# Kernel tuning notes

Hardware: AMD Instinct MI355X
Metric: run time of the kernel (lower is better)

Reference implementation:

```python
import jax, jax.numpy as jnp
import numpy as np

NPOINT, RADIUS, NSAMPLE = 1024, 0.2, 32
BN_EPS = 1e-5


def fps(xyz_bn3, npoint):
    # xyz_bn3: (B, N, 3) -> (B, npoint) int32 indices; starts from point 0 like the CUDA ext.
    def one(x):
        N = x.shape[0]
        def step(carry, _):
            dist, last = carry
            d = jnp.sum((x - x[last]) ** 2, axis=-1)
            dist = jnp.minimum(dist, d)
            nxt = jnp.argmax(dist).astype(jnp.int32)
            return (dist, nxt), nxt
        init = (jnp.full((N,), 1e10, dtype=x.dtype), jnp.int32(0))
        _, rest = jax.lax.scan(step, init, None, length=npoint - 1)
        return jnp.concatenate([jnp.zeros((1,), jnp.int32), rest])
    return jax.vmap(one)(xyz_bn3)


def ball_query(radius, nsample, xyz, new_xyz):
    # xyz: (B, N, 3), new_xyz: (B, S, 3) -> (B, S, nsample) int32
    # First nsample points within radius; pad slots with the first found index.
    N = xyz.shape[1]
    d2 = jnp.sum((new_xyz[:, :, None, :] - xyz[:, None, :, :]) ** 2, axis=-1)  # (B,S,N)
    ar = jnp.arange(N, dtype=jnp.int32)
    cand = jnp.where(d2 <= radius * radius, ar, N)
    idx = jnp.sort(cand, axis=-1)[..., :nsample]
    first = idx[..., :1]
    return jnp.where(idx == N, first, idx)


def group(features, idx):
    # features: (B, C, N), idx: (B, S, K) -> (B, C, S, K)
    return jax.vmap(lambda f, i: f[:, i])(features, idx)


def conv_bn_relu(x, w, b, g, bt, rm, rv):
    # x: (B, Cin, S, K); 1x1 conv + eval-mode BatchNorm + ReLU
    y = jnp.einsum('oc,bcsk->bosk', w, x) + b[:, None, None]
    y = g[:, None, None] * (y - rm[:, None, None]) * jax.lax.rsqrt(rv[:, None, None] + BN_EPS) + bt[:, None, None]
    return jax.nn.relu(y)


def setup_inputs() -> dict:
    key = jax.random.key(0)
    ks = jax.random.split(key, 16)
    B, N, D = 8, 4096, 64
    mlp = [64, 64, 128]
    cin = 3 + D
    inp = {
        'xyz': jax.random.uniform(ks[0], (B, 3, N), dtype=jnp.float32),
        'points': jax.random.normal(ks[1], (B, D, N), dtype=jnp.float32),
    }
    last = cin
    kidx = 2
    for i, co in enumerate(mlp):
        inp[f'w{i}'] = jax.random.normal(ks[kidx], (co, last), dtype=jnp.float32) * (1.0 / np.sqrt(last)); kidx += 1
        inp[f'b{i}'] = jax.random.normal(ks[kidx], (co,), dtype=jnp.float32) * 0.01; kidx += 1
        inp[f'g{i}'] = jax.random.uniform(ks[kidx], (co,), dtype=jnp.float32) + 0.5; kidx += 1
        inp[f'bt{i}'] = jax.random.normal(ks[kidx], (co,), dtype=jnp.float32) * 0.01; kidx += 1
        inp[f'rm{i}'] = jnp.zeros((co,), dtype=jnp.float32)
        inp[f'rv{i}'] = jnp.ones((co,), dtype=jnp.float32)
        last = co
    return inp


def reference(xyz, points, w0, b0, g0, bt0, rm0, rv0, w1, b1, g1, bt1, rm1, rv1, w2, b2, g2, bt2, rm2, rv2):
    xyz_t = jnp.transpose(xyz, (0, 2, 1))  # (B, N, 3)
    fps_idx = fps(xyz_t, NPOINT)  # (B, S)
    new_xyz = jax.vmap(lambda f, i: f[:, i])(xyz, fps_idx)  # (B, 3, S)
    idx = ball_query(RADIUS, NSAMPLE, xyz_t, jnp.transpose(new_xyz, (0, 2, 1)))  # (B, S, K)
    grouped_xyz = group(xyz, idx) - new_xyz[..., None]  # (B, 3, S, K)
    grouped_pts = group(points, idx)  # (B, D, S, K)
    feat = jnp.concatenate([grouped_xyz, grouped_pts], axis=1)  # (B, 3+D, S, K)
    feat = conv_bn_relu(feat, w0, b0, g0, bt0, rm0, rv0)
    feat = conv_bn_relu(feat, w1, b1, g1, bt1, rm1, rv1)
    feat = conv_bn_relu(feat, w2, b2, g2, bt2, rm2, rv2)
    new_features = jnp.max(feat, axis=-1)  # (B, 128, S)
    return new_xyz, new_features
```

## Files before the change

kernel.cpp:

```cpp
#include <hip/hip_runtime.h>
#include <cstdint>
#include <cstddef>

#define NPOINT 1024
#define NSAMPLE 32
#define BATCH 8
#define NPTS 4096
#define DFEAT 64
#define CIN 67
#define C1 64
#define C2 64
#define C3 128
#define BN_EPS 1e-5f

__device__ __forceinline__ float wave64_max_bcast(float v) {
    int x;
    x = __builtin_amdgcn_update_dpp(0, __float_as_int(v), 0x111, 0xf, 0xf, true);
    v = fmaxf(v, __int_as_float(x));
    x = __builtin_amdgcn_update_dpp(0, __float_as_int(v), 0x112, 0xf, 0xf, true);
    v = fmaxf(v, __int_as_float(x));
    x = __builtin_amdgcn_update_dpp(0, __float_as_int(v), 0x114, 0xf, 0xf, true);
    v = fmaxf(v, __int_as_float(x));
    x = __builtin_amdgcn_update_dpp(0, __float_as_int(v), 0x118, 0xf, 0xf, true);
    v = fmaxf(v, __int_as_float(x));
    x = __builtin_amdgcn_update_dpp(0, __float_as_int(v), 0x142, 0xf, 0xf, true);
    v = fmaxf(v, __int_as_float(x));
    x = __builtin_amdgcn_update_dpp(0, __float_as_int(v), 0x143, 0xf, 0xf, true);
    v = fmaxf(v, __int_as_float(x));
    return __int_as_float(__builtin_amdgcn_readlane(__float_as_int(v), 63));
}

__global__ __launch_bounds__(512) void fps_kernel(const float* __restrict__ xyz,
                                                  float* __restrict__ dout) {
    const int b = blockIdx.x;
    const float* xb = xyz + (size_t)b * 3 * NPTS;
    float* ox = dout + (size_t)b * 3 * NPOINT;

    __shared__ float sx[NPTS], sy[NPTS], sz[NPTS];
    __shared__ unsigned long long redk[2][8];

    const int t = threadIdx.x;
    const int wv = t >> 6, lane = t & 63;
    for (int j = t; j < NPTS; j += 512) {
        sx[j] = xb[j];
        sy[j] = xb[NPTS + j];
        sz[j] = xb[2 * NPTS + j];
    }
    __syncthreads();

    constexpr int PT = NPTS / 512;
    float px[PT], py[PT], pz[PT], dist[PT];
    const int base = t * PT;
#pragma unroll
    for (int u = 0; u < PT; ++u) {
        px[u] = sx[base + u];
        py[u] = sy[base + u];
        pz[u] = sz[base + u];
        dist[u] = 1e10f;
    }

    int last = 0;
    float o0x = 0.f, o0y = 0.f, o0z = 0.f;
    float o1x = 0.f, o1y = 0.f, o1z = 0.f;

    for (int s = 1; s < NPOINT; ++s) {
        const float cx = sx[last], cy = sy[last], cz = sz[last];
        if (s - 1 == t)       { o0x = cx; o0y = cy; o0z = cz; }
        if (s - 1 == t + 512) { o1x = cx; o1y = cy; o1z = cz; }

        float bv = 0.0f;
#pragma unroll
        for (int u = 0; u < PT; ++u) {
            float dx = __fsub_rn(px[u], cx);
            float dy = __fsub_rn(py[u], cy);
            float dz = __fsub_rn(pz[u], cz);
            float d = __fadd_rn(__fadd_rn(__fmul_rn(dx, dx), __fmul_rn(dy, dy)),
                                __fmul_rn(dz, dz));
            float nd = fminf(dist[u], d);
            dist[u] = nd;
            bv = fmaxf(bv, nd);
        }
        const float wmax = wave64_max_bcast(bv);
        int li = 0;
        if (bv == wmax) {
#pragma unroll
            for (int u = PT - 1; u >= 0; --u)
                if (dist[u] == wmax) li = base + u;
        }
        const unsigned long long m = __ballot(bv == wmax);
        const int fl = __builtin_ctzll(m);
        const int wbi = __builtin_amdgcn_readlane(li, fl);

        if ((t & 63) == 0) {
            redk[s & 1][wv] =
                ((unsigned long long)__float_as_uint(wmax) << 32) |
                (unsigned)(0xFFFFFFFFu - (unsigned)wbi);
        }
        __syncthreads();
        unsigned long long gk = redk[s & 1][0];
#pragma unroll
        for (int w = 1; w < 8; ++w) {
            unsigned long long k2 = redk[s & 1][w];
            if (k2 > gk) gk = k2;
        }
        last = (int)(0xFFFFFFFFu - (unsigned)(gk & 0xFFFFFFFFull));
    }

    {
        const float cx = sx[last], cy = sy[last], cz = sz[last];
        if (t == 511) { o1x = cx; o1y = cy; o1z = cz; }
    }

    ox[t] = o0x;
    ox[NPOINT + t] = o0y;
    ox[2 * NPOINT + t] = o0z;
    ox[512 + t] = o1x;
    ox[NPOINT + 512 + t] = o1y;
    ox[2 * NPOINT + 512 + t] = o1z;
}

__global__ __launch_bounds__(256) void transpose_pts(const float* __restrict__ pts,
                                                     float* __restrict__ ptsT) {
    __shared__ float tile[64][65];
    const int b = blockIdx.x / (NPTS / 64);
    const int n0 = (blockIdx.x % (NPTS / 64)) * 64;
    const int t = threadIdx.x;
    const int nl = t & 63, cq = t >> 6;
    const float* pb = pts + (size_t)b * DFEAT * NPTS;
#pragma unroll
    for (int i = 0; i < 16; ++i) {
        int c = i * 4 + cq;
        tile[c][nl] = pb[(size_t)c * NPTS + n0 + nl];
    }
    __syncthreads();
    float* ob = ptsT + (size_t)b * NPTS * DFEAT;
    const int cl = t & 63, nq = t >> 6;
#pragma unroll
    for (int i = 0; i < 16; ++i) {
        int n = i * 4 + nq;
        ob[(size_t)(n0 + n) * DFEAT + cl] = tile[cl][n];
    }
}

__global__ __launch_bounds__(256) void ballquery_kernel(const float* __restrict__ xyz,
                                                        const float* __restrict__ dout,
                                                        int* __restrict__ idx) {
    const int wv = threadIdx.x >> 6, lane = threadIdx.x & 63;
    const int sg = blockIdx.x * 4 + wv;
    const int b = sg / NPOINT, s = sg % NPOINT;
    const float* xb = xyz + (size_t)b * 3 * NPTS;
    const float* nx = dout + (size_t)b * 3 * NPOINT;
    const float cx = nx[s], cy = nx[NPOINT + s], cz = nx[2 * NPOINT + s];
    int* ob = idx + (size_t)sg * NSAMPLE;
    const float r2 = 0.04f;

    int cnt = 0;
    int first = -1;
    for (int tch = 0; tch < NPTS / 64 && cnt < NSAMPLE; ++tch) {
        const int j = tch * 64 + lane;
        float dx = __fsub_rn(cx, xb[j]);
        float dy = __fsub_rn(cy, xb[NPTS + j]);
        float dz = __fsub_rn(cz, xb[2 * NPTS + j]);
        float d2 = __fadd_rn(__fadd_rn(__fmul_rn(dx, dx), __fmul_rn(dy, dy)),
                             __fmul_rn(dz, dz));
        unsigned long long mask = __ballot(d2 <= r2);
        while (mask && cnt < NSAMPLE) {
            int bit = __builtin_ctzll(mask);
            int pj = tch * 64 + bit;
            if (cnt == 0) first = pj;
            if (lane == 0) ob[cnt] = pj;
            cnt++;
            mask &= mask - 1;
        }
    }
    if (lane == 0) {
        for (int r = cnt; r < NSAMPLE; ++r) ob[r] = first;
    }
}

template <int TRANSPOSED>
__global__ __launch_bounds__(256) void mlp_kernel(
    const float* __restrict__ xyz, const float* __restrict__ pts,
    const int* __restrict__ idx, const float* __restrict__ dnew,
    const float* __restrict__ w0, const float* __restrict__ b0,
    const float* __restrict__ g0, const float* __restrict__ bt0,
    const float* __restrict__ rm0, const float* __restrict__ rv0,
    const float* __restrict__ w1, const float* __restrict__ b1,
    const float* __restrict__ g1, const float* __restrict__ bt1,
    const float* __restrict__ rm1, const float* __restrict__ rv1,
    const float* __restrict__ w2, const float* __restrict__ b2,
    const float* __restrict__ g2, const float* __restrict__ bt2,
    const float* __restrict__ rm2, const float* __restrict__ rv2,
    float* __restrict__ outf) {
    __shared__ float ylds[64][256];
    const int t = threadIdx.x;
    const int k = t & 31, sl = t >> 5;
    const int b = blockIdx.x >> 7;
    const int s = (blockIdx.x & 127) * 8 + sl;
    const int p = idx[((size_t)(b * NPOINT + s)) * NSAMPLE + k];

    const float* xb = xyz + (size_t)b * 3 * NPTS;
    const float* nx = dnew + (size_t)b * 3 * NPOINT;

    float x[CIN];
    x[0] = xb[p] - nx[s];
    x[1] = xb[NPTS + p] - nx[NPOINT + s];
    x[2] = xb[2 * NPTS + p] - nx[2 * NPOINT + s];
    if (TRANSPOSED) {
        const float* pb = pts + ((size_t)b * NPTS + p) * DFEAT;
#pragma unroll
        for (int c = 0; c < DFEAT; ++c) x[3 + c] = pb[c];
    } else {
        const float* pb = pts + (size_t)b * DFEAT * NPTS + p;
#pragma unroll
        for (int c = 0; c < DFEAT; ++c) x[3 + c] = pb[(size_t)c * NPTS];
    }

    for (int o = 0; o < C1; ++o) {
        const float* wr = w0 + o * CIN;
        float a0 = 0.f, a1 = 0.f, a2 = 0.f, a3 = 0.f;
#pragma unroll
        for (int c = 0; c < 64; c += 4) {
            a0 = fmaf(wr[c], x[c], a0);
            a1 = fmaf(wr[c + 1], x[c + 1], a1);
            a2 = fmaf(wr[c + 2], x[c + 2], a2);
            a3 = fmaf(wr[c + 3], x[c + 3], a3);
        }
        a0 = fmaf(wr[64], x[64], a0);
        a1 = fmaf(wr[65], x[65], a1);
        a2 = fmaf(wr[66], x[66], a2);
        float acc = (a0 + a1) + (a2 + a3);
        float sc = g0[o] * rsqrtf(rv0[o] + BN_EPS);
        float y = fmaf(sc, acc + b0[o] - rm0[o], bt0[o]);
        ylds[o][t] = fmaxf(y, 0.f);
    }
    __syncthreads();
    float x1[C1];
#pragma unroll
    for (int c = 0; c < C1; ++c) x1[c] = ylds[c][t];
    __syncthreads();

    for (int o = 0; o < C2; ++o) {
        const float* wr = w1 + o * C1;
        float a0 = 0.f, a1 = 0.f, a2 = 0.f, a3 = 0.f;
#pragma unroll
        for (int c = 0; c < C1; c += 4) {
            a0 = fmaf(wr[c], x1[c], a0);
            a1 = fmaf(wr[c + 1], x1[c + 1], a1);
            a2 = fmaf(wr[c + 2], x1[c + 2], a2);
            a3 = fmaf(wr[c + 3], x1[c + 3], a3);
        }
        float acc = (a0 + a1) + (a2 + a3);
        float sc = g1[o] * rsqrtf(rv1[o] + BN_EPS);
        float y = fmaf(sc, acc + b1[o] - rm1[o], bt1[o]);
        ylds[o][t] = fmaxf(y, 0.f);
    }
    __syncthreads();
    float x2[C2];
#pragma unroll
    for (int c = 0; c < C2; ++c) x2[c] = ylds[c][t];

    float* ob = outf + (size_t)b * C3 * NPOINT;
    for (int o = 0; o < C3; ++o) {
        const float* wr = w2 + o * C2;
        float a0 = 0.f, a1 = 0.f, a2 = 0.f, a3 = 0.f;
#pragma unroll
        for (int c = 0; c < C2; c += 4) {
            a0 = fmaf(wr[c], x2[c], a0);
            a1 = fmaf(wr[c + 1], x2[c + 1], a1);
            a2 = fmaf(wr[c + 2], x2[c + 2], a2);
            a3 = fmaf(wr[c + 3], x2[c + 3], a3);
        }
        float acc = (a0 + a1) + (a2 + a3);
        float sc = g2[o] * rsqrtf(rv2[o] + BN_EPS);
        float y = fmaf(sc, acc + b2[o] - rm2[o], bt2[o]);
        float v = fmaxf(y, 0.f);
#pragma unroll
        for (int m = 16; m >= 1; m >>= 1) v = fmaxf(v, __shfl_xor(v, m, 32));
        if (k == 0) ob[(size_t)o * NPOINT + s] = v;
    }
}

extern "C" void kernel_launch(void* const* d_in, const int* in_sizes, int n_in,
                              void* d_out, int out_size, void* d_ws, size_t ws_size,
                              hipStream_t stream) {
    const float* xyz = (const float*)d_in[0];
    const float* pts = (const float*)d_in[1];
    const float* w0 = (const float*)d_in[2];
    const float* b0 = (const float*)d_in[3];
    const float* g0 = (const float*)d_in[4];
    const float* bt0 = (const float*)d_in[5];
    const float* rm0 = (const float*)d_in[6];
    const float* rv0 = (const float*)d_in[7];
    const float* w1 = (const float*)d_in[8];
    const float* b1 = (const float*)d_in[9];
    const float* g1 = (const float*)d_in[10];
    const float* bt1 = (const float*)d_in[11];
    const float* rm1 = (const float*)d_in[12];
    const float* rv1 = (const float*)d_in[13];
    const float* w2 = (const float*)d_in[14];
    const float* b2 = (const float*)d_in[15];
    const float* g2 = (const float*)d_in[16];
    const float* bt2 = (const float*)d_in[17];
    const float* rm2 = (const float*)d_in[18];
    const float* rv2 = (const float*)d_in[19];

    float* out = (float*)d_out;
    float* outf = out + (size_t)BATCH * 3 * NPOINT;

    const size_t idx_bytes = (size_t)BATCH * NPOINT * NSAMPLE * sizeof(int);
    const size_t idx_pad = (idx_bytes + 255) & ~(size_t)255;
    const size_t ptsT_bytes = (size_t)BATCH * NPTS * DFEAT * sizeof(float);
    int* idx = (int*)d_ws;
    float* ptsT = (float*)((char*)d_ws + idx_pad);
    const bool useT = ws_size >= idx_pad + ptsT_bytes;

    fps_kernel<<<BATCH, 512, 0, stream>>>(xyz, out);
    if (useT) transpose_pts<<<BATCH * (NPTS / 64), 256, 0, stream>>>(pts, ptsT);
    ballquery_kernel<<<BATCH * NPOINT / 4, 256, 0, stream>>>(xyz, out, idx);
    if (useT) {
        mlp_kernel<1><<<BATCH * NPOINT / 8, 256, 0, stream>>>(
            xyz, ptsT, idx, out, w0, b0, g0, bt0, rm0, rv0, w1, b1, g1, bt1, rm1,
            rv1, w2, b2, g2, bt2, rm2, rv2, outf);
    } else {
        mlp_kernel<0><<<BATCH * NPOINT / 8, 256, 0, stream>>>(
            xyz, pts, idx, out, w0, b0, g0, bt0, rm0, rv0, w1, b1, g1, bt1, rm1,
            rv1, w2, b2, g2, bt2, rm2, rv2, outf);
    }
}
```

Measured before the change: 958.7 us.

## Precompute layer-1 point-feature projection per point and simplify ball query and max

The first conv layer is split: the 64-channel feature part is multiplied by the weights once per source point in a new kernel, replacing the transpose. The MLP kernel then gathers a 64-wide precomputed row and adds only the 3 xyz terms, cutting layer-1 FLOPs by about 32x since each point is reused across many neighborhoods. Ball query now writes in parallel using popcount prefix ranks instead of a serial per-bit loop. The final max over samples is taken on pre-BN accumulators with sign handling, so BN and ReLU run once per channel, and uses DPP row ops in place of shuffles.

Result: faster. 926.4 us (-3.4%).

```diff
diff --git a/kernel.cpp b/kernel.cpp
--- a/kernel.cpp
+++ b/kernel.cpp
@@ -30,6 +30,21 @@
     return __int_as_float(__builtin_amdgcn_readlane(__float_as_int(v), 63));
 }
 
+__device__ __forceinline__ float max32_lane31(float v) {
+    int iv = __float_as_int(v), x;
+    x = __builtin_amdgcn_update_dpp(iv, iv, 0x111, 0xf, 0xf, false);
+    v = fmaxf(v, __int_as_float(x)); iv = __float_as_int(v);
+    x = __builtin_amdgcn_update_dpp(iv, iv, 0x112, 0xf, 0xf, false);
+    v = fmaxf(v, __int_as_float(x)); iv = __float_as_int(v);
+    x = __builtin_amdgcn_update_dpp(iv, iv, 0x114, 0xf, 0xf, false);
+    v = fmaxf(v, __int_as_float(x)); iv = __float_as_int(v);
+    x = __builtin_amdgcn_update_dpp(iv, iv, 0x118, 0xf, 0xf, false);
+    v = fmaxf(v, __int_as_float(x)); iv = __float_as_int(v);
+    x = __builtin_amdgcn_update_dpp(iv, iv, 0x142, 0xf, 0xf, false);
+    v = fmaxf(v, __int_as_float(x));
+    return v;
+}
+
 __global__ __launch_bounds__(512) void fps_kernel(const float* __restrict__ xyz,
                                                   float* __restrict__ dout) {
     const int b = blockIdx.x;
@@ -40,7 +55,7 @@
     __shared__ unsigned long long redk[2][8];
 
     const int t = threadIdx.x;
-    const int wv = t >> 6, lane = t & 63;
+    const int wv = t >> 6;
     for (int j = t; j < NPTS; j += 512) {
         sx[j] = xb[j];
         sy[j] = xb[NPTS + j];
@@ -119,26 +134,41 @@
     ox[2 * NPOINT + 512 + t] = o1z;
 }
 
-__global__ __launch_bounds__(256) void transpose_pts(const float* __restrict__ pts,
-                                                     float* __restrict__ ptsT) {
-    __shared__ float tile[64][65];
-    const int b = blockIdx.x / (NPTS / 64);
-    const int n0 = (blockIdx.x % (NPTS / 64)) * 64;
+__global__ __launch_bounds__(256) void layer1_pts_kernel(
+    const float* __restrict__ pts, const float* __restrict__ w0,
+    float* __restrict__ A) {
+    __shared__ float sp[64][65];
+    __shared__ float sw[64][65];
+    const int b = blockIdx.x >> 6;
+    const int n0 = (blockIdx.x & 63) * 64;
     const int t = threadIdx.x;
-    const int nl = t & 63, cq = t >> 6;
+    const int tn = t & 63, tq = t >> 6;
     const float* pb = pts + (size_t)b * DFEAT * NPTS;
 #pragma unroll
     for (int i = 0; i < 16; ++i) {
-        int c = i * 4 + cq;
-        tile[c][nl] = pb[(size_t)c * NPTS + n0 + nl];
-    }
-    __syncthreads();
-    float* ob = ptsT + (size_t)b * NPTS * DFEAT;
-    const int cl = t & 63, nq = t >> 6;
+        int c = i * 4 + tq;
+        sp[c][tn] = pb[(size_t)c * NPTS + n0 + tn];
+    }
 #pragma unroll
     for (int i = 0; i < 16; ++i) {
-        int n = i * 4 + nq;
-        ob[(size_t)(n0 + n) * DFEAT + cl] = tile[cl][n];
+        int o = i * 4 + tq;
+        sw[o][tn] = w0[o * CIN + 3 + tn];
+    }
+    __syncthreads();
+
+    float* An = A + ((size_t)b * NPTS + n0 + tn) * DFEAT;
+#pragma unroll
+    for (int i = 0; i < 16; ++i) {
+        const int o = tq * 16 + i;
+        float a0 = 0.f, a1 = 0.f, a2 = 0.f, a3 = 0.f;
+#pragma unroll
+        for (int c = 0; c < 64; c += 4) {
+            a0 = fmaf(sw[o][c], sp[c][tn], a0);
+            a1 = fmaf(sw[o][c + 1], sp[c + 1][tn], a1);
+            a2 = fmaf(sw[o][c + 2], sp[c + 2][tn], a2);
+            a3 = fmaf(sw[o][c + 3], sp[c + 3][tn], a3);
+        }
+        An[o] = (a0 + a1) + (a2 + a3);
     }
 }
 
@@ -153,6 +183,7 @@
     const float cx = nx[s], cy = nx[NPOINT + s], cz = nx[2 * NPOINT + s];
     int* ob = idx + (size_t)sg * NSAMPLE;
     const float r2 = 0.04f;
+    const unsigned long long lmask_lt = ((unsigned long long)1 << lane) - 1;
 
     int cnt = 0;
     int first = -1;
@@ -163,25 +194,26 @@
         float dz = __fsub_rn(cz, xb[2 * NPTS + j]);
         float d2 = __fadd_rn(__fadd_rn(__fmul_rn(dx, dx), __fmul_rn(dy, dy)),
                              __fmul_rn(dz, dz));
-        unsigned long long mask = __ballot(d2 <= r2);
-        while (mask && cnt < NSAMPLE) {
-            int bit = __builtin_ctzll(mask);
-            int pj = tch * 64 + bit;
-            if (cnt == 0) first = pj;
-            if (lane == 0) ob[cnt] = pj;
-            cnt++;
-            mask &= mask - 1;
-        }
+        const bool in = (d2 <= r2);
+        const unsigned long long mask = __ballot(in);
+        if (first < 0 && mask)
+            first = tch * 64 + __builtin_ctzll(mask);
+        if (in) {
+            const int pos = cnt + __builtin_popcountll(mask & lmask_lt);
+            if (pos < NSAMPLE) ob[pos] = j;
+        }
+        cnt += __builtin_popcountll(mask);
     }
     if (lane == 0) {
         for (int r = cnt; r < NSAMPLE; ++r) ob[r] = first;
     }
 }
 
-template <int TRANSPOSED>
+template <int MODE>
 __global__ __launch_bounds__(256) void mlp_kernel(
     const float* __restrict__ xyz, const float* __restrict__ pts,
-    const int* __restrict__ idx, const float* __restrict__ dnew,
+    const float* __restrict__ A, const int* __restrict__ idx,
+    const float* __restrict__ dnew,
     const float* __restrict__ w0, const float* __restrict__ b0,
     const float* __restrict__ g0, const float* __restrict__ bt0,
     const float* __restrict__ rm0, const float* __restrict__ rv0,
@@ -202,37 +234,51 @@
     const float* xb = xyz + (size_t)b * 3 * NPTS;
     const float* nx = dnew + (size_t)b * 3 * NPOINT;
 
-    float x[CIN];
-    x[0] = xb[p] - nx[s];
-    x[1] = xb[NPTS + p] - nx[NPOINT + s];
-    x[2] = xb[2 * NPTS + p] - nx[2 * NPOINT + s];
-    if (TRANSPOSED) {
-        const float* pb = pts + ((size_t)b * NPTS + p) * DFEAT;
-#pragma unroll
-        for (int c = 0; c < DFEAT; ++c) x[3 + c] = pb[c];
+    const float gx = xb[p] - nx[s];
+    const float gy = xb[NPTS + p] - nx[NPOINT + s];
+    const float gz = xb[2 * NPTS + p] - nx[2 * NPOINT + s];
+
+    if (MODE == 1) {
+        const float* Arow = A + ((size_t)b * NPTS + p) * DFEAT;
+        for (int og = 0; og < C1; og += 4) {
+            const float4 av = *(const float4*)(Arow + og);
+#pragma unroll
+            for (int u = 0; u < 4; ++u) {
+                const int o = og + u;
+                const float avu = (u == 0) ? av.x : (u == 1) ? av.y
+                                 : (u == 2) ? av.z : av.w;
+                const float* wr = w0 + o * CIN;
+                float acc = fmaf(wr[0], gx,
+                            fmaf(wr[1], gy, fmaf(wr[2], gz, avu)));
+                float sc = g0[o] * rsqrtf(rv0[o] + BN_EPS);
+                float y = fmaf(sc, acc + b0[o] - rm0[o], bt0[o]);
+                ylds[o][t] = fmaxf(y, 0.f);
+            }
+        }
     } else {
+        float x[CIN];
+        x[0] = gx; x[1] = gy; x[2] = gz;
         const float* pb = pts + (size_t)b * DFEAT * NPTS + p;
 #pragma unroll
         for (int c = 0; c < DFEAT; ++c) x[3 + c] = pb[(size_t)c * NPTS];
-    }
-
-    for (int o = 0; o < C1; ++o) {
-        const float* wr = w0 + o * CIN;
-        float a0 = 0.f, a1 = 0.f, a2 = 0.f, a3 = 0.f;
-#pragma unroll
-        for (int c = 0; c < 64; c += 4) {
-            a0 = fmaf(wr[c], x[c], a0);
-            a1 = fmaf(wr[c + 1], x[c + 1], a1);
-            a2 = fmaf(wr[c + 2], x[c + 2], a2);
-            a3 = fmaf(wr[c + 3], x[c + 3], a3);
-        }
-        a0 = fmaf(wr[64], x[64], a0);
-        a1 = fmaf(wr[65], x[65], a1);
-        a2 = fmaf(wr[66], x[66], a2);
-        float acc = (a0 + a1) + (a2 + a3);
-        float sc = g0[o] * rsqrtf(rv0[o] + BN_EPS);
-        float y = fmaf(sc, acc + b0[o] - rm0[o], bt0[o]);
-        ylds[o][t] = fmaxf(y, 0.f);
+        for (int o = 0; o < C1; ++o) {
+            const float* wr = w0 + o * CIN;
+            float a0 = 0.f, a1 = 0.f, a2 = 0.f, a3 = 0.f;
+#pragma unroll
+            for (int c = 0; c < 64; c += 4) {
+                a0 = fmaf(wr[c], x[c], a0);
+                a1 = fmaf(wr[c + 1], x[c + 1], a1);
+                a2 = fmaf(wr[c + 2], x[c + 2], a2);
+                a3 = fmaf(wr[c + 3], x[c + 3], a3);
+            }
+            a0 = fmaf(wr[64], x[64], a0);
+            a1 = fmaf(wr[65], x[65], a1);
+            a2 = fmaf(wr[66], x[66], a2);
+            float acc = (a0 + a1) + (a2 + a3);
+            float sc = g0[o] * rsqrtf(rv0[o] + BN_EPS);
+            float y = fmaf(sc, acc + b0[o] - rm0[o], bt0[o]);
+            ylds[o][t] = fmaxf(y, 0.f);
+        }
     }
     __syncthreads();
     float x1[C1];
@@ -273,11 +319,13 @@
         }
         float acc = (a0 + a1) + (a2 + a3);
         float sc = g2[o] * rsqrtf(rv2[o] + BN_EPS);
-        float y = fmaf(sc, acc + b2[o] - rm2[o], bt2[o]);
-        float v = fmaxf(y, 0.f);
-#pragma unroll
-        for (int m = 16; m >= 1; m >>= 1) v = fmaxf(v, __shfl_xor(v, m, 32));
-        if (k == 0) ob[(size_t)o * NPOINT + s] = v;
+        float key = (sc >= 0.f) ? acc : -acc;
+        float mred = max32_lane31(key);
+        if (k == 31) {
+            float asel = (sc >= 0.f) ? mred : -mred;
+            float y = fmaf(sc, asel + b2[o] - rm2[o], bt2[o]);
+            ob[(size_t)o * NPOINT + s] = fmaxf(y, 0.f);
+        }
     }
 }
 
@@ -310,21 +358,21 @@
 
     const size_t idx_bytes = (size_t)BATCH * NPOINT * NSAMPLE * sizeof(int);
     const size_t idx_pad = (idx_bytes + 255) & ~(size_t)255;
-    const size_t ptsT_bytes = (size_t)BATCH * NPTS * DFEAT * sizeof(float);
+    const size_t A_bytes = (size_t)BATCH * NPTS * DFEAT * sizeof(float);
     int* idx = (int*)d_ws;
-    float* ptsT = (float*)((char*)d_ws + idx_pad);
-    const bool useT = ws_size >= idx_pad + ptsT_bytes;
+    float* A = (float*)((char*)d_ws + idx_pad);
+    const bool useA = ws_size >= idx_pad + A_bytes;
 
     fps_kernel<<<BATCH, 512, 0, stream>>>(xyz, out);
-    if (useT) transpose_pts<<<BATCH * (NPTS / 64), 256, 0, stream>>>(pts, ptsT);
+    if (useA) layer1_pts_kernel<<<BATCH * 64, 256, 0, stream>>>(pts, w0, A);
     ballquery_kernel<<<BATCH * NPOINT / 4, 256, 0, stream>>>(xyz, out, idx);
-    if (useT) {
+    if (useA) {
         mlp_kernel<1><<<BATCH * NPOINT / 8, 256, 0, stream>>>(
-            xyz, ptsT, idx, out, w0, b0, g0, bt0, rm0, rv0, w1, b1, g1, bt1, rm1,
-            rv1, w2, b2, g2, bt2, rm2, rv2, outf);
+            xyz, pts, A, idx, out, w0, b0, g0, bt0, rm0, rv0, w1, b1, g1, bt1,
+            rm1, rv1, w2, b2, g2, bt2, rm2, rv2, outf);
     } else {
         mlp_kernel<0><<<BATCH * NPOINT / 8, 256, 0, stream>>>(
-            xyz, pts, idx, out, w0, b0, g0, bt0, rm0, rv0, w1, b1, g1, bt1, rm1,
-            rv1, w2, b2, g2, bt2, rm2, rv2, outf);
-    }
-}
+            xyz, pts, A, idx, out, w0, b0, g0, bt0, rm0, rv0, w1, b1, g1, bt1,
+            rm1, rv1, w2, b2, g2, bt2, rm2, rv2, outf);
+    }
+}
```
